# Kernel tuning notes

Measured on AMD Instinct MI355X. Metric: run time of the kernel, lower is better.

Reference implementation:

```python
import jax, jax.numpy as jnp
import numpy as np

B, S, H, DH = 8, 1024, 16, 64
D = H * DH  # d_model = 1024
M_ALPHA = -1e9


def setup_inputs() -> dict:
    key = jax.random.key(0)
    ks = jax.random.split(key, 11)
    scale = 1.0 / np.sqrt(D)
    x = jax.random.normal(ks[0], (B, S, D), dtype=jnp.float32)
    # 0/1 padding mask, shape [B, S, 1] (1 = masked position)
    mask = (jax.random.uniform(ks[1], (B, S, 1)) < 0.25).astype(jnp.float32)
    mk = lambda k: jax.random.normal(k, (D, D), dtype=jnp.float32) * scale
    return {
        "x": x,
        "mask": mask,
        "wq_w": mk(ks[2]), "wq_b": jnp.zeros((D,), jnp.float32),
        "wk_w": mk(ks[3]), "wk_b": jnp.zeros((D,), jnp.float32),
        "wv_w": mk(ks[4]), "wv_b": jnp.zeros((D,), jnp.float32),
        "wo_w": mk(ks[5]), "wo_b": jnp.zeros((D,), jnp.float32),
    }


def _split_heads(t):
    # [B, S, D] -> [B, H, S, DH]
    return t.reshape(B, S, H, DH).transpose(0, 2, 1, 3)


def reference(x, mask, wq_w, wq_b, wk_w, wk_b, wv_w, wv_b, wo_w, wo_b):
    q = _split_heads(x @ wq_w + wq_b)  # [B,H,S,DH]
    k = _split_heads(x @ wk_w + wk_b)
    v = _split_heads(x @ wv_w + wv_b)

    logits = jnp.einsum("bhqd,bhkd->bhqk", q, k) / jnp.sqrt(
        jnp.asarray(DH, jnp.float32))
    qk_values = logits  # pre-mask scaled logits (temperature == 0.0 -> no-op)

    # QK mask path: mask [B,S,1] -> tile to [B,S,S] rows (m[b,i,j] = mask[b,i]),
    # then symmetrize (square) -> mask[b,i] + mask[b,j], clamp at 1.
    m = mask[:, :, 0]                               # [B,S]
    mask_qk = jnp.minimum(1.0, m[:, :, None] + m[:, None, :])  # [B,S,S]
    logits = logits + mask_qk[:, None, :, :] * M_ALPHA

    attn = jax.nn.softmax(logits, axis=-1)          # [B,H,S,S]
    z = jnp.einsum("bhqk,bhkd->bhqd", attn, v)      # [B,H,S,DH]
    z = z.transpose(0, 2, 1, 3).reshape(B, S, D)
    out = z @ wo_w + wo_b
    return (out, attn, qk_values, q, k, v)
```

## Files before the change

kernel.cpp:

```cpp
#include <hip/hip_runtime.h>
#include <hip/hip_bf16.h>
#include <stdint.h>

#define BB 8
#define SS 1024
#define HH 16
#define DHD 64
#define DD 1024

typedef __attribute__((ext_vector_type(8))) short bf16x8;
typedef __attribute__((ext_vector_type(4))) float f32x4;

__device__ __forceinline__ unsigned short f2bf(float f) {
  unsigned u = __builtin_bit_cast(unsigned, f);
  u += 0x7fffu + ((u >> 16) & 1u);
  return (unsigned short)(u >> 16);
}

__device__ __forceinline__ unsigned swz(unsigned a) { return a ^ ((a >> 3) & 0x70u); }

#define GLOAD16(gp, lp)                                                        \
  __builtin_amdgcn_global_load_lds(                                            \
      (const __attribute__((address_space(1))) unsigned int*)(gp),             \
      (__attribute__((address_space(3))) unsigned int*)(lp), 16, 0, 0)

#define MFMA16(a, b, c) __builtin_amdgcn_mfma_f32_16x16x32_bf16(a, b, c, 0, 0, 0)

__global__ __launch_bounds__(256) void cvt_x_kernel(const float* __restrict__ x,
                                                    unsigned short* __restrict__ xb) {
  int i = blockIdx.x * 256 + threadIdx.x;
  float4 v = ((const float4*)x)[i];
  ushort4 o;
  o.x = f2bf(v.x); o.y = f2bf(v.y); o.z = f2bf(v.z); o.w = f2bf(v.w);
  ((ushort4*)xb)[i] = o;
}

__global__ __launch_bounds__(256) void transpose_w_kernel(
    const float* __restrict__ w0, const float* __restrict__ w1,
    const float* __restrict__ w2, const float* __restrict__ w3,
    unsigned short* __restrict__ o0, unsigned short* __restrict__ o1,
    unsigned short* __restrict__ o2, unsigned short* __restrict__ o3) {
  __shared__ float tile[32][33];
  const float* src; unsigned short* dst;
  if (blockIdx.z == 0)      { src = w0; dst = o0; }
  else if (blockIdx.z == 1) { src = w1; dst = o1; }
  else if (blockIdx.z == 2) { src = w2; dst = o2; }
  else                      { src = w3; dst = o3; }
  int n0 = blockIdx.x * 32, k0 = blockIdx.y * 32;
  int tx = threadIdx.x, ty = threadIdx.y;
#pragma unroll
  for (int j = 0; j < 32; j += 8)
    tile[ty + j][tx] = src[(size_t)(k0 + ty + j) * DD + n0 + tx];
  __syncthreads();
#pragma unroll
  for (int j = 0; j < 32; j += 8)
    dst[(size_t)(n0 + ty + j) * DD + k0 + tx] = f2bf(tile[tx][ty + j]);
}

__global__ __launch_bounds__(256) void proj_gemm_kernel(
    const unsigned short* __restrict__ xb,
    const unsigned short* __restrict__ wqt, const unsigned short* __restrict__ wkt,
    const unsigned short* __restrict__ wvt,
    const float* __restrict__ bq, const float* __restrict__ bk, const float* __restrict__ bv,
    float* __restrict__ qo, float* __restrict__ ko, float* __restrict__ vo,
    unsigned short* __restrict__ qb, unsigned short* __restrict__ kbf,
    unsigned short* __restrict__ vt) {
  __shared__ __align__(128) unsigned short smem[2 * 128 * 64];
  unsigned short* As = smem;
  unsigned short* Bs = smem + 128 * 64;
  const int tid = threadIdx.x, lane = tid & 63, w = tid >> 6;
  const int wr = (w >> 1) * 64, wc = (w & 1) * 64;
  const int m0 = blockIdx.x * 128;
  const int mat = blockIdx.y >> 3;
  const int n0 = (blockIdx.y & 7) * 128;
  const unsigned short* Bg = (mat == 0) ? wqt : (mat == 1) ? wkt : wvt;
  const float* bias = (mat == 0) ? bq : (mat == 1) ? bk : bv;

  f32x4 acc[4][4];
  f32x4 z4 = {0.f, 0.f, 0.f, 0.f};
#pragma unroll
  for (int i = 0; i < 4; ++i)
#pragma unroll
    for (int j = 0; j < 4; ++j) acc[i][j] = z4;

  for (int kt = 0; kt < 1024; kt += 64) {
    __syncthreads();
#pragma unroll
    for (int i = 0; i < 4; ++i) {
      unsigned obase = (unsigned)(w * 4096 + i * 1024);
      unsigned a = swz(obase + (unsigned)lane * 16);
      GLOAD16((const char*)xb + ((size_t)(m0 + (int)(a >> 7)) * 1024 + kt) * 2 + (a & 127),
              (char*)As + obase);
      GLOAD16((const char*)Bg + ((size_t)(n0 + (int)(a >> 7)) * 1024 + kt) * 2 + (a & 127),
              (char*)Bs + obase);
    }
    __syncthreads();
#pragma unroll
    for (int ks = 0; ks < 2; ++ks) {
      bf16x8 af[4], bfr[4];
#pragma unroll
      for (int mi = 0; mi < 4; ++mi) {
        unsigned a = (unsigned)((wr + mi * 16 + (lane & 15)) * 128 + ks * 64 + ((lane >> 4) * 16));
        af[mi] = *(const bf16x8*)((const char*)As + swz(a));
      }
#pragma unroll
      for (int ni = 0; ni < 4; ++ni) {
        unsigned a = (unsigned)((wc + ni * 16 + (lane & 15)) * 128 + ks * 64 + ((lane >> 4) * 16));
        bfr[ni] = *(const bf16x8*)((const char*)Bs + swz(a));
      }
#pragma unroll
      for (int mi = 0; mi < 4; ++mi)
#pragma unroll
        for (int ni = 0; ni < 4; ++ni)
          acc[mi][ni] = MFMA16(af[mi], bfr[ni], acc[mi][ni]);
    }
  }

  float* fo = (mat == 0) ? qo : (mat == 1) ? ko : vo;
  __syncthreads();
  unsigned short* T = smem;

#pragma unroll
  for (int mi = 0; mi < 4; ++mi)
#pragma unroll
    for (int ni = 0; ni < 4; ++ni) {
      int col = n0 + wc + ni * 16 + (lane & 15);
      float bs = bias[col];
#pragma unroll
      for (int r = 0; r < 4; ++r) {
        int row = m0 + wr + mi * 16 + ((lane >> 4) << 2) + r;
        float v = acc[mi][ni][r] + bs;
        int b = row >> 10, s = row & 1023, h = col >> 6, dh = col & 63;
        size_t bh = (size_t)(b * HH + h);
        __builtin_nontemporal_store(v, &fo[(bh * SS + s) * DHD + dh]);
        if (mat == 2) {
          int sl = wr + mi * 16 + ((lane >> 4) << 2) + r;
          int dl = wc + ni * 16 + (lane & 15);
          T[dl * 128 + (sl ^ ((dl & 7) << 4))] = f2bf(v);
        } else if (mat == 0) {
          qb[(bh * SS + s) * DHD + dh] = f2bf(v * 0.125f);
        } else {
          kbf[(bh * SS + s) * DHD + dh] = f2bf(v);
        }
      }
    }

  if (mat == 2) {
    __syncthreads();
    int row = tid >> 1;
    int half = tid & 1;
    int colg = n0 + row;
    int h2 = colg >> 6, dh2 = colg & 63;
    int b = m0 >> 10;
    int sg0 = (m0 & 1023) + half * 64;
    unsigned short* dst = vt + (((size_t)(b * HH + h2)) * DHD + dh2) * SS + sg0;
#pragma unroll
    for (int j = 0; j < 8; ++j) {
      int sc = half * 64 + j * 8;
      bf16x8 vv = *(const bf16x8*)&T[row * 128 + (sc ^ ((row & 7) << 4))];
      *(bf16x8*)(dst + j * 8) = vv;
    }
  }
}

__global__ __launch_bounds__(256) void attn_kernel(
    const unsigned short* __restrict__ qb, const unsigned short* __restrict__ kb,
    const unsigned short* __restrict__ vt, const float* __restrict__ mask,
    float* __restrict__ qk_out, float* __restrict__ attn_out,
    unsigned short* __restrict__ zb) {
  __shared__ __align__(128) unsigned short kbuf[64 * 64];
  __shared__ __align__(128) unsigned short vbuf[64 * 64];
  __shared__ __align__(128) unsigned short pbuf[4][16 * 64];
  __shared__ __align__(16) float mbuf[SS];

  const int tid = threadIdx.x, lane = tid & 63, w = tid >> 6;
  const int fid = blockIdx.x;
  const int bh = fid & 127, qt = fid >> 7;
  const int b = bh >> 4, h = bh & 15;
  const int r0 = qt * 64 + w * 16;
  const int q15 = lane & 15, G = lane >> 4;

  ((float4*)mbuf)[tid] = ((const float4*)(mask + (size_t)b * SS))[tid];
  __syncthreads();

  bf16x8 aq[2];
  {
    const unsigned short* p = qb + (size_t)bh * SS * DHD + (size_t)(r0 + q15) * DHD + G * 8;
    aq[0] = *(const bf16x8*)p;
    aq[1] = *(const bf16x8*)(p + 32);
  }
  const float mq = mbuf[r0 + q15];

  const unsigned short* kbase = kb + (size_t)bh * SS * DHD;
  const char* vbase = (const char*)(vt + (size_t)bh * DHD * SS);
  float* qkb = qk_out + (size_t)bh * SS * SS;
  float* atb = attn_out + (size_t)bh * SS * SS;
  float* qrow = qkb + (size_t)(r0 + q15) * SS;
  float* arow = atb + (size_t)(r0 + q15) * SS;

  float m_run = -INFINITY, l_run = 0.f;

  for (int kt = 0; kt < 16; ++kt) {
    int k0 = kt * 64;
    __syncthreads();
#pragma unroll
    for (int i = 0; i < 2; ++i) {
      unsigned obase = (unsigned)(w * 2048 + i * 1024);
      unsigned a = swz(obase + (unsigned)lane * 16);
      GLOAD16((const char*)(kbase + (size_t)k0 * 64) + a, (char*)kbuf + obase);
    }
    __syncthreads();
    f32x4 sm[4];
#pragma unroll
    for (int ct = 0; ct < 4; ++ct) {
      f32x4 acc = {0.f, 0.f, 0.f, 0.f};
#pragma unroll
      for (int ks = 0; ks < 2; ++ks) {
        unsigned a = (unsigned)((ct * 16 + q15) * 128 + ks * 64 + G * 16);
        bf16x8 bk = *(const bf16x8*)((const char*)kbuf + swz(a));
        acc = MFMA16(bk, aq[ks], acc);
      }
      int c0 = k0 + ct * 16 + G * 4;
      __builtin_nontemporal_store(acc, (f32x4*)(qrow + c0));
      float4 mk4 = *(const float4*)(mbuf + c0);
#pragma unroll
      for (int r = 0; r < 4; ++r) {
        float t = fminf(mq + ((const float*)&mk4)[r], 1.f);
        sm[ct][r] = acc[r] + t * (-1.0e9f);
      }
    }
    float mx = sm[0][0];
#pragma unroll
    for (int ct = 0; ct < 4; ++ct)
#pragma unroll
      for (int r = 0; r < 4; ++r) mx = fmaxf(mx, sm[ct][r]);
    mx = fmaxf(mx, __shfl_xor(mx, 16, 64));
    mx = fmaxf(mx, __shfl_xor(mx, 32, 64));
    float m_new = fmaxf(m_run, mx);
    float es = 0.f;
#pragma unroll
    for (int ct = 0; ct < 4; ++ct)
#pragma unroll
      for (int r = 0; r < 4; ++r) es += __expf(sm[ct][r] - m_new);
    es += __shfl_xor(es, 16, 64);
    es += __shfl_xor(es, 32, 64);
    l_run = l_run * __expf(m_run - m_new) + es;
    m_run = m_new;
  }

  const float inv_l = 1.0f / l_run;

  f32x4 zacc[4];
#pragma unroll
  for (int dt = 0; dt < 4; ++dt) zacc[dt] = (f32x4){0.f, 0.f, 0.f, 0.f};

  unsigned short* pw = pbuf[w];
  const unsigned pswz = (unsigned)((q15 & 14) << 3);

  for (int kt = 0; kt < 16; ++kt) {
    int k0 = kt * 64;
    __syncthreads();
#pragma unroll
    for (int i = 0; i < 2; ++i) {
      unsigned obase = (unsigned)(w * 2048 + i * 1024);
      unsigned a = swz(obase + (unsigned)lane * 16);
      GLOAD16((const char*)(kbase + (size_t)k0 * 64) + a, (char*)kbuf + obase);
      GLOAD16(vbase + (size_t)(a >> 7) * (SS * 2) + (size_t)k0 * 2 + (a & 127),
              (char*)vbuf + obase);
    }
    __syncthreads();
#pragma unroll
    for (int ct = 0; ct < 4; ++ct) {
      f32x4 acc = {0.f, 0.f, 0.f, 0.f};
#pragma unroll
      for (int ks = 0; ks < 2; ++ks) {
        unsigned a = (unsigned)((ct * 16 + q15) * 128 + ks * 64 + G * 16);
        bf16x8 bk = *(const bf16x8*)((const char*)kbuf + swz(a));
        acc = MFMA16(bk, aq[ks], acc);
      }
      int c0 = k0 + ct * 16 + G * 4;
      float4 mk4 = *(const float4*)(mbuf + c0);
      f32x4 pn;
#pragma unroll
      for (int r = 0; r < 4; ++r) {
        float t = fminf(mq + ((const float*)&mk4)[r], 1.f);
        pn[r] = __expf(acc[r] + t * (-1.0e9f) - m_run) * inv_l;
      }
      __builtin_nontemporal_store(pn, (f32x4*)(arow + c0));
      unsigned u0 = (unsigned)f2bf(pn[0]) | ((unsigned)f2bf(pn[1]) << 16);
      unsigned u1 = (unsigned)f2bf(pn[2]) | ((unsigned)f2bf(pn[3]) << 16);
      uint2 pkd = {u0, u1};
      *(uint2*)((char*)pw + (((unsigned)(q15 * 128 + ct * 32 + G * 8)) ^ pswz)) = pkd;
    }
    bf16x8 pa[2];
#pragma unroll
    for (int ks = 0; ks < 2; ++ks)
      pa[ks] = *(const bf16x8*)((char*)pw + (((unsigned)(q15 * 128 + ks * 64 + G * 16)) ^ pswz));
#pragma unroll
    for (int dt = 0; dt < 4; ++dt) {
#pragma unroll
      for (int ks = 0; ks < 2; ++ks) {
        unsigned av = (unsigned)((dt * 16 + q15) * 128 + ks * 64 + G * 16);
        bf16x8 bv = *(const bf16x8*)((const char*)vbuf + swz(av));
        zacc[dt] = MFMA16(pa[ks], bv, zacc[dt]);
      }
    }
  }

#pragma unroll
  for (int dt = 0; dt < 4; ++dt)
#pragma unroll
    for (int r = 0; r < 4; ++r) {
      int srow = r0 + G * 4 + r;
      int dcol = dt * 16 + q15;
      zb[((size_t)b * SS + srow) * DD + h * 64 + dcol] = f2bf(zacc[dt][r]);
    }
}

__global__ __launch_bounds__(256) void out_gemm_kernel(
    const unsigned short* __restrict__ zb, const unsigned short* __restrict__ wot,
    const float* __restrict__ bo, float* __restrict__ outp) {
  __shared__ __align__(128) unsigned short As[128 * 64];
  __shared__ __align__(128) unsigned short Bs[128 * 64];
  const int tid = threadIdx.x, lane = tid & 63, w = tid >> 6;
  const int wr = (w >> 1) * 64, wc = (w & 1) * 64;
  const int m0 = blockIdx.x * 128;
  const int n0 = blockIdx.y * 128;

  f32x4 acc[4][4];
  f32x4 z4 = {0.f, 0.f, 0.f, 0.f};
#pragma unroll
  for (int i = 0; i < 4; ++i)
#pragma unroll
    for (int j = 0; j < 4; ++j) acc[i][j] = z4;

  for (int kt = 0; kt < 1024; kt += 64) {
    __syncthreads();
#pragma unroll
    for (int i = 0; i < 4; ++i) {
      unsigned obase = (unsigned)(w * 4096 + i * 1024);
      unsigned a = swz(obase + (unsigned)lane * 16);
      GLOAD16((const char*)zb + ((size_t)(m0 + (int)(a >> 7)) * 1024 + kt) * 2 + (a & 127),
              (char*)As + obase);
      GLOAD16((const char*)wot + ((size_t)(n0 + (int)(a >> 7)) * 1024 + kt) * 2 + (a & 127),
              (char*)Bs + obase);
    }
    __syncthreads();
#pragma unroll
    for (int ks = 0; ks < 2; ++ks) {
      bf16x8 af[4], bfr[4];
#pragma unroll
      for (int mi = 0; mi < 4; ++mi) {
        unsigned a = (unsigned)((wr + mi * 16 + (lane & 15)) * 128 + ks * 64 + ((lane >> 4) * 16));
        af[mi] = *(const bf16x8*)((const char*)As + swz(a));
      }
#pragma unroll
      for (int ni = 0; ni < 4; ++ni) {
        unsigned a = (unsigned)((wc + ni * 16 + (lane & 15)) * 128 + ks * 64 + ((lane >> 4) * 16));
        bfr[ni] = *(const bf16x8*)((const char*)Bs + swz(a));
      }
#pragma unroll
      for (int mi = 0; mi < 4; ++mi)
#pragma unroll
        for (int ni = 0; ni < 4; ++ni)
          acc[mi][ni] = MFMA16(af[mi], bfr[ni], acc[mi][ni]);
    }
  }
#pragma unroll
  for (int mi = 0; mi < 4; ++mi)
#pragma unroll
    for (int ni = 0; ni < 4; ++ni) {
      int col = n0 + wc + ni * 16 + (lane & 15);
      float bs = bo[col];
#pragma unroll
      for (int r = 0; r < 4; ++r) {
        int row = m0 + wr + mi * 16 + ((lane >> 4) << 2) + r;
        __builtin_nontemporal_store(acc[mi][ni][r] + bs, &outp[(size_t)row * DD + col]);
      }
    }
}

extern "C" void kernel_launch(void* const* d_in, const int* in_sizes, int n_in,
                              void* d_out, int out_size, void* d_ws, size_t ws_size,
                              hipStream_t stream) {
  const float* x    = (const float*)d_in[0];
  const float* mask = (const float*)d_in[1];
  const float* wq_w = (const float*)d_in[2];
  const float* wq_b = (const float*)d_in[3];
  const float* wk_w = (const float*)d_in[4];
  const float* wk_b = (const float*)d_in[5];
  const float* wv_w = (const float*)d_in[6];
  const float* wv_b = (const float*)d_in[7];
  const float* wo_w = (const float*)d_in[8];
  const float* wo_b = (const float*)d_in[9];

  float* outp = (float*)d_out;
  float* attn = outp + (size_t)8388608;
  float* qk   = attn + (size_t)134217728;
  float* qo   = qk + (size_t)134217728;
  float* ko   = qo + (size_t)8388608;
  float* vo   = ko + (size_t)8388608;

  char* ws = (char*)d_ws;
  unsigned short* xb  = (unsigned short*)(ws + 0);
  unsigned short* wqt = (unsigned short*)(ws + 16777216);
  unsigned short* wkt = (unsigned short*)(ws + 18874368);
  unsigned short* wvt = (unsigned short*)(ws + 20971520);
  unsigned short* wot = (unsigned short*)(ws + 23068672);
  unsigned short* qb  = (unsigned short*)(ws + 25165824);
  unsigned short* kb  = (unsigned short*)(ws + 41943040);
  unsigned short* vt  = (unsigned short*)(ws + 58720256);
  unsigned short* zb  = (unsigned short*)(ws + 75497472);

  cvt_x_kernel<<<8192, 256, 0, stream>>>(x, xb);
  transpose_w_kernel<<<dim3(32, 32, 4), dim3(32, 8), 0, stream>>>(
      wq_w, wk_w, wv_w, wo_w, wqt, wkt, wvt, wot);
  proj_gemm_kernel<<<dim3(64, 24), 256, 0, stream>>>(
      xb, wqt, wkt, wvt, wq_b, wk_b, wv_b, qo, ko, vo, qb, kb, vt);
  attn_kernel<<<2048, 256, 0, stream>>>(qb, kb, vt, mask, qk, attn, zb);
  out_gemm_kernel<<<dim3(64, 8), 256, 0, stream>>>(zb, wot, wo_b, outp);
}
```

Baseline: 523.1 us.

## Read K, V and mask directly from global memory instead of LDS staging

The attention kernel no longer stages K and V tiles and the mask row through shared memory with global_load_lds and block-wide barriers. Each wave now loads its MFMA operands straight from global memory, relying on L1/L2 caching. This removes the per-tile __syncthreads pairs and shrinks LDS use, which may raise occupancy. The cost is that every wave fetches the same K/V data redundantly, with less coalesced 16-byte loads and exposed global latency.

```diff
diff --git a/kernel.cpp b/kernel.cpp
--- a/kernel.cpp
+++ b/kernel.cpp
@@ -168,10 +168,7 @@
     const unsigned short* __restrict__ vt, const float* __restrict__ mask,
     float* __restrict__ qk_out, float* __restrict__ attn_out,
     unsigned short* __restrict__ zb) {
-  __shared__ __align__(128) unsigned short kbuf[64 * 64];
-  __shared__ __align__(128) unsigned short vbuf[64 * 64];
   __shared__ __align__(128) unsigned short pbuf[4][16 * 64];
-  __shared__ __align__(16) float mbuf[SS];
 
   const int tid = threadIdx.x, lane = tid & 63, w = tid >> 6;
   const int fid = blockIdx.x;
@@ -180,49 +177,36 @@
   const int r0 = qt * 64 + w * 16;
   const int q15 = lane & 15, G = lane >> 4;
 
-  ((float4*)mbuf)[tid] = ((const float4*)(mask + (size_t)b * SS))[tid];
-  __syncthreads();
-
   bf16x8 aq[2];
   {
     const unsigned short* p = qb + (size_t)bh * SS * DHD + (size_t)(r0 + q15) * DHD + G * 8;
     aq[0] = *(const bf16x8*)p;
     aq[1] = *(const bf16x8*)(p + 32);
   }
-  const float mq = mbuf[r0 + q15];
+  const float* mrow = mask + (size_t)b * SS;
+  const float mq = mrow[r0 + q15];
 
   const unsigned short* kbase = kb + (size_t)bh * SS * DHD;
-  const char* vbase = (const char*)(vt + (size_t)bh * DHD * SS);
-  float* qkb = qk_out + (size_t)bh * SS * SS;
-  float* atb = attn_out + (size_t)bh * SS * SS;
-  float* qrow = qkb + (size_t)(r0 + q15) * SS;
-  float* arow = atb + (size_t)(r0 + q15) * SS;
+  const unsigned short* vbase = vt + (size_t)bh * DHD * SS;
+  float* qrow = qk_out + (size_t)bh * SS * SS + (size_t)(r0 + q15) * SS;
+  float* arow = attn_out + (size_t)bh * SS * SS + (size_t)(r0 + q15) * SS;
 
   float m_run = -INFINITY, l_run = 0.f;
 
   for (int kt = 0; kt < 16; ++kt) {
     int k0 = kt * 64;
-    __syncthreads();
-#pragma unroll
-    for (int i = 0; i < 2; ++i) {
-      unsigned obase = (unsigned)(w * 2048 + i * 1024);
-      unsigned a = swz(obase + (unsigned)lane * 16);
-      GLOAD16((const char*)(kbase + (size_t)k0 * 64) + a, (char*)kbuf + obase);
-    }
-    __syncthreads();
     f32x4 sm[4];
 #pragma unroll
     for (int ct = 0; ct < 4; ++ct) {
       f32x4 acc = {0.f, 0.f, 0.f, 0.f};
 #pragma unroll
       for (int ks = 0; ks < 2; ++ks) {
-        unsigned a = (unsigned)((ct * 16 + q15) * 128 + ks * 64 + G * 16);
-        bf16x8 bk = *(const bf16x8*)((const char*)kbuf + swz(a));
+        bf16x8 bk = *(const bf16x8*)(kbase + (size_t)(k0 + ct * 16 + q15) * 64 + ks * 32 + G * 8);
         acc = MFMA16(bk, aq[ks], acc);
       }
       int c0 = k0 + ct * 16 + G * 4;
       __builtin_nontemporal_store(acc, (f32x4*)(qrow + c0));
-      float4 mk4 = *(const float4*)(mbuf + c0);
+      float4 mk4 = *(const float4*)(mrow + c0);
 #pragma unroll
       for (int r = 0; r < 4; ++r) {
         float t = fminf(mq + ((const float*)&mk4)[r], 1.f);
@@ -259,27 +243,16 @@
 
   for (int kt = 0; kt < 16; ++kt) {
     int k0 = kt * 64;
-    __syncthreads();
-#pragma unroll
-    for (int i = 0; i < 2; ++i) {
-      unsigned obase = (unsigned)(w * 2048 + i * 1024);
-      unsigned a = swz(obase + (unsigned)lane * 16);
-      GLOAD16((const char*)(kbase + (size_t)k0 * 64) + a, (char*)kbuf + obase);
-      GLOAD16(vbase + (size_t)(a >> 7) * (SS * 2) + (size_t)k0 * 2 + (a & 127),
-              (char*)vbuf + obase);
-    }
-    __syncthreads();
 #pragma unroll
     for (int ct = 0; ct < 4; ++ct) {
       f32x4 acc = {0.f, 0.f, 0.f, 0.f};
 #pragma unroll
       for (int ks = 0; ks < 2; ++ks) {
-        unsigned a = (unsigned)((ct * 16 + q15) * 128 + ks * 64 + G * 16);
-        bf16x8 bk = *(const bf16x8*)((const char*)kbuf + swz(a));
+        bf16x8 bk = *(const bf16x8*)(kbase + (size_t)(k0 + ct * 16 + q15) * 64 + ks * 32 + G * 8);
         acc = MFMA16(bk, aq[ks], acc);
       }
       int c0 = k0 + ct * 16 + G * 4;
-      float4 mk4 = *(const float4*)(mbuf + c0);
+      float4 mk4 = *(const float4*)(mrow + c0);
       f32x4 pn;
 #pragma unroll
       for (int r = 0; r < 4; ++r) {
@@ -300,8 +273,7 @@
     for (int dt = 0; dt < 4; ++dt) {
 #pragma unroll
       for (int ks = 0; ks < 2; ++ks) {
-        unsigned av = (unsigned)((dt * 16 + q15) * 128 + ks * 64 + G * 16);
-        bf16x8 bv = *(const bf16x8*)((const char*)vbuf + swz(av));
+        bf16x8 bv = *(const bf16x8*)(vbase + (size_t)(dt * 16 + q15) * SS + k0 + ks * 32 + G * 8);
         zacc[dt] = MFMA16(pa[ks], bv, zacc[dt]);
       }
     }
```

Result: slower. 561.5 us (+7.3%).
